# Performance work log

Hardware: AMD Instinct MI355X
Metric: run time of the kernel (lower is better)

## Reference

```python
import jax, jax.numpy as jnp
import numpy as np

GRAY_W = jnp.array([0.2989, 0.587, 0.114], dtype=jnp.float32)  # torchvision rgb_to_grayscale


def bilinear_sample(img, sx, sy):
    """img: [..., H, W]; sx, sy: [Ho, Wo] source pixel coords; zero padding (grid_sample bilinear)."""
    H, W = img.shape[-2], img.shape[-1]
    x0 = jnp.floor(sx)
    y0 = jnp.floor(sy)
    wx1 = sx - x0
    wy1 = sy - y0
    wx0 = 1.0 - wx1
    wy0 = 1.0 - wy1

    def gather(xi, yi):
        valid = (xi >= 0) & (xi <= W - 1) & (yi >= 0) & (yi <= H - 1)
        xc = jnp.clip(xi, 0, W - 1).astype(jnp.int32)
        yc = jnp.clip(yi, 0, H - 1).astype(jnp.int32)
        return img[..., yc, xc] * valid.astype(img.dtype)

    return (gather(x0, y0) * (wy0 * wx0) + gather(x0 + 1.0, y0) * (wy0 * wx1)
            + gather(x0, y0 + 1.0) * (wy1 * wx0) + gather(x0 + 1.0, y0 + 1.0) * (wy1 * wx1))


def forward(adv_patch, lab_batch, img_size):
    B, L = lab_batch.shape[0], lab_batch.shape[1]
    N, S = B * L, img_size
    key = jax.random.key(42)
    kb, kc, ks, kn, ka, ksc, kp = jax.random.split(key, 7)

    # Resize (bilinear, half-pixel centers). All N expanded copies are identical at this
    # point, so resize + color-jitter once on the single patch, then broadcast (same math).
    p = jax.image.resize(adv_patch, (3, S, S), method="bilinear")

    # ColorJitter: one factor per transform per call, applied to the whole batch.
    b = jax.random.uniform(kb, (), minval=0.8, maxval=1.1)
    c = jax.random.uniform(kc, (), minval=0.8, maxval=1.1)
    s = jax.random.uniform(ks, (), minval=0.8, maxval=1.1)
    p = p * b                                                    # brightness
    p = c * p + (1.0 - c) * jnp.einsum('chw,c->hw', p, GRAY_W).mean()   # contrast
    p = s * p + (1.0 - s) * jnp.einsum('chw,c->hw', p, GRAY_W)[None]    # saturation

    # Uniform noise in [-1,1] * noise_factor, per element of the full [N,3,S,S] batch.
    batch = p[None] + 0.15 * jax.random.uniform(kn, (N, 3, S, S), minval=-1.0, maxval=1.0)

    # RandomAffine(degrees=(-45,45), scale=(0.1,0.16)): rotation+scale about image
    # center, one sample per call; inverse map, shared [S,S] grid for all N images.
    theta = jnp.deg2rad(jax.random.uniform(ka, (), minval=-45.0, maxval=45.0))
    sc = jax.random.uniform(ksc, (), minval=0.1, maxval=0.16)
    ctr = (S - 1) / 2.0
    xs = jnp.arange(S, dtype=jnp.float32) - ctr
    dy, dx = jnp.meshgrid(xs, xs, indexing='ij')
    cos_t, sin_t = jnp.cos(theta), jnp.sin(theta)
    sx = (cos_t * dx + sin_t * dy) / sc + ctr
    sy = (-sin_t * dx + cos_t * dy) / sc + ctr
    batch = bilinear_sample(batch, sx, sy)

    # RandomPerspective(distortion_scale=0.6, p=1.0): corners pulled inward by random
    # integer offsets in [0, 0.6*half]; solve homography T with T(endpoint)=startpoint
    # (output->source map), shared for the whole batch.
    dmax = int(0.6 * (S // 2))
    r = jax.random.randint(kp, (8,), 0, dmax + 1).astype(jnp.float32)
    w = jnp.float32(S - 1)
    end = jnp.stack([jnp.stack([r[0], r[1]]),
                     jnp.stack([w - r[2], r[3]]),
                     jnp.stack([w - r[4], w - r[5]]),
                     jnp.stack([r[6], w - r[7]])])  # [4,2] endpoints (tl,tr,br,bl)
    start = jnp.array([[0.0, 0.0], [1.0, 0.0], [1.0, 1.0], [0.0, 1.0]], jnp.float32) * w
    ex, ey = end[:, 0], end[:, 1]
    px, py = start[:, 0], start[:, 1]
    z, o = jnp.zeros(4, jnp.float32), jnp.ones(4, jnp.float32)
    A = jnp.concatenate([
        jnp.stack([ex, ey, o, z, z, z, -px * ex, -px * ey], axis=1),
        jnp.stack([z, z, z, ex, ey, o, -py * ex, -py * ey], axis=1)], axis=0)  # [8,8]
    rhs = jnp.concatenate([px, py])
    h = jnp.linalg.solve(A, rhs)
    xo = jnp.arange(S, dtype=jnp.float32) + 0.5  # torchvision perspective grid offset
    yo_g, xo_g = jnp.meshgrid(xo, xo, indexing='ij')
    den = h[6] * xo_g + h[7] * yo_g + 1.0
    psx = (h[0] * xo_g + h[1] * yo_g + h[2]) / den - 0.5
    psy = (h[3] * xo_g + h[4] * yo_g + h[5]) / den - 0.5
    batch = bilinear_sample(batch, psx, psy)

    return jnp.clip(batch, 0.0, 0.99).reshape(B, L, 3, S, S)


def setup_inputs() -> dict:
    key = jax.random.key(0)
    k1, k2 = jax.random.split(key)
    return {
        "adv_patch": jax.random.uniform(k1, (3, 300, 300), dtype=jnp.float32),
        "lab_batch": jax.random.normal(k2, (8, 14, 5), dtype=jnp.float32),
        "img_size": 416,
    }


def reference(adv_patch, lab_batch, img_size):
    return forward(adv_patch, lab_batch, img_size)
```

## Files before the change

### kernel.cpp

```cpp
#include <hip/hip_runtime.h>
#include <cstdint>
#include <cstring>
#include <cmath>

__host__ __device__ static inline uint32_t rotl32(uint32_t x, int r) {
  return (x << r) | (x >> (32 - r));
}

__host__ __device__ static inline void tf2x32(uint32_t k0, uint32_t k1,
                                              uint32_t c0, uint32_t c1,
                                              uint32_t& o0, uint32_t& o1) {
  const uint32_t ks2 = 0x1BD11BDAu ^ k0 ^ k1;
  uint32_t x0 = c0 + k0;
  uint32_t x1 = c1 + k1;
#define TF_QR(r) { x0 += x1; x1 = rotl32(x1, (r)); x1 ^= x0; }
  TF_QR(13) TF_QR(15) TF_QR(26) TF_QR(6)
  x0 += k1;  x1 += ks2 + 1u;
  TF_QR(17) TF_QR(29) TF_QR(16) TF_QR(24)
  x0 += ks2; x1 += k0 + 2u;
  TF_QR(13) TF_QR(15) TF_QR(26) TF_QR(6)
  x0 += k0;  x1 += k1 + 3u;
  TF_QR(17) TF_QR(29) TF_QR(16) TF_QR(24)
  x0 += k1;  x1 += ks2 + 4u;
  TF_QR(13) TF_QR(15) TF_QR(26) TF_QR(6)
  x0 += ks2; x1 += k0 + 5u;
#undef TF_QR
  o0 = x0; o1 = x1;
}

__host__ __device__ static inline uint32_t tf_bits32(uint32_t k0, uint32_t k1, uint32_t i) {
  uint32_t a, b;
  tf2x32(k0, k1, 0u, i, a, b);
  return a ^ b;
}

__device__ static inline float noise_from_bits(uint32_t bits) {
  uint32_t fb = (bits >> 9) | 0x3f800000u;
  float f = __uint_as_float(fb) - 1.0f;
  float v = f * 2.0f - 1.0f;
  v = fmaxf(-1.0f, v);
  return 0.15f * v;
}


__global__ void __launch_bounds__(256)
k_resize(const float* __restrict__ src, float* __restrict__ p1,
         double* __restrict__ part, float bmul, int S, int inS, int SS) {
  __shared__ double sh[256];
  int t = blockIdx.x * 256 + threadIdx.x;
  double g = 0.0;
  if (t < SS) {
    int y = t / S, x = t - y * S;
    float fs = (float)inS / (float)S;
    float fy = ((float)y + 0.5f) * fs - 0.5f;
    float fx = ((float)x + 0.5f) * fs - 0.5f;
    float y0f = floorf(fy), x0f = floorf(fx);
    float ty = fy - y0f, tx = fx - x0f;
    int y0 = (int)y0f, x0 = (int)x0f;
    int y1 = y0 + 1, x1 = x0 + 1;
    y0 = min(max(y0, 0), inS - 1); y1 = min(max(y1, 0), inS - 1);
    x0 = min(max(x0, 0), inS - 1); x1 = min(max(x1, 0), inS - 1);
    float w00 = (1.f - ty) * (1.f - tx), w01 = (1.f - ty) * tx;
    float w10 = ty * (1.f - tx),         w11 = ty * tx;
    float rgb[3];
    for (int c = 0; c < 3; ++c) {
      const float* pc = src + (size_t)c * inS * inS;
      float v = pc[y0 * inS + x0] * w00 + pc[y0 * inS + x1] * w01 +
                pc[y1 * inS + x0] * w10 + pc[y1 * inS + x1] * w11;
      v *= bmul;
      p1[(size_t)c * SS + t] = v;
      rgb[c] = v;
    }
    g = (double)(0.2989f * rgb[0] + 0.587f * rgb[1] + 0.114f * rgb[2]);
  }
  sh[threadIdx.x] = g;
  __syncthreads();
  for (int s2 = 128; s2 > 0; s2 >>= 1) {
    if (threadIdx.x < s2) sh[threadIdx.x] += sh[threadIdx.x + s2];
    __syncthreads();
  }
  if (threadIdx.x == 0) part[blockIdx.x] = sh[0];
}

__global__ void __launch_bounds__(256)
k_batch1c(const float* __restrict__ p1, float* __restrict__ b1,
          const double* __restrict__ part, int nb,
          float cc, float ssat,
          uint32_t kn0, uint32_t kn1, int S, int SS, int blo, int bw, int bwp,
          float cos_t, float sin_t, float sc, float ctr) {
  __shared__ double sh[256];
  double a = 0.0;
  for (int i = threadIdx.x; i < nb; i += 256) a += part[i];
  sh[threadIdx.x] = a;
  __syncthreads();
  for (int s2 = 128; s2 > 0; s2 >>= 1) {
    if (threadIdx.x < s2) sh[threadIdx.x] += sh[threadIdx.x + s2];
    __syncthreads();
  }
  float m = (float)(sh[0] / (double)SS);

  int pix = blockIdx.x * 256 + threadIdx.x;
  if (pix >= bw * bw) return;
  int px = pix % bw;
  int py = pix / bw;
  int n  = blockIdx.y;

  int xt = blo + px, yt = blo + py;
  float dx = (float)xt - ctr, dy = (float)yt - ctr;
  float sx = (cos_t * dx + sin_t * dy) / sc + ctr;
  float sy = (-sin_t * dx + cos_t * dy) / sc + ctr;
  float x0f = floorf(sx), y0f = floorf(sy);
  float wx1 = sx - x0f, wy1 = sy - y0f;
  float wx0 = 1.f - wx1, wy0 = 1.f - wy1;
  float Wm1 = (float)(S - 1);
  float xtf[4] = {x0f, x0f + 1.f, x0f, x0f + 1.f};
  float ytf[4] = {y0f, y0f, y0f + 1.f, y0f + 1.f};
  float wt[4]  = {wy0 * wx0, wy0 * wx1, wy1 * wx0, wy1 * wx1};
  float acc[3] = {0.f, 0.f, 0.f};
  uint32_t nbase = (uint32_t)(n * 3) * (uint32_t)SS;
  float omc = 1.0f - cc, oms = 1.0f - ssat;
#pragma unroll
  for (int u = 0; u < 4; ++u) {
    bool valid = (xtf[u] >= 0.f) && (xtf[u] <= Wm1) && (ytf[u] >= 0.f) && (ytf[u] <= Wm1);
    if (!valid) continue;
    int ix = (int)xtf[u], iy = (int)ytf[u];
    int sp = iy * S + ix;
    float r = p1[sp], g = p1[SS + sp], b = p1[2 * SS + sp];
    float r2 = cc * r + omc * m;
    float g2 = cc * g + omc * m;
    float b2 = cc * b + omc * m;
    float gray = 0.2989f * r2 + 0.587f * g2 + 0.114f * b2;
    float pfv[3];
    pfv[0] = ssat * r2 + oms * gray;
    pfv[1] = ssat * g2 + oms * gray;
    pfv[2] = ssat * b2 + oms * gray;
    uint32_t idx0 = nbase + (uint32_t)sp;
#pragma unroll
    for (int c = 0; c < 3; ++c) {
      uint32_t bits = tf_bits32(kn0, kn1, idx0 + (uint32_t)(c * SS));
      acc[c] += wt[u] * (pfv[c] + noise_from_bits(bits));
    }
  }
#pragma unroll
  for (int c = 0; c < 3; ++c)
    b1[(((size_t)n * 3 + c) * bw + py) * bwp + px] = acc[c];
}

__global__ void __launch_bounds__(256)
k_out8(const float* __restrict__ b1, float4* __restrict__ out,
       int S, int X8, int blo, int bhi, int bw, int bwp, int N,
       float h0, float h1, float h2, float h3, float h4, float h5, float h6, float h7) {
  int tid = blockIdx.x * 256 + threadIdx.x;
  int total = N * S * X8;
  if (tid >= total) return;
  int x8 = tid % X8;
  int t2 = tid / X8;
  int y  = t2 % S;
  int n  = t2 / S;

  int X4 = X8 * 2;
  float yo  = (float)y + 0.5f;
  float xo0 = (float)(x8 * 8) + 0.5f;
  float xo7 = xo0 + 7.0f;

  float den0 = h6 * xo0 + h7 * yo + 1.0f;
  float den7 = h6 * xo7 + h7 * yo + 1.0f;
  float psx0 = (h0 * xo0 + h1 * yo + h2) / den0 - 0.5f;
  float psy0 = (h3 * xo0 + h4 * yo + h5) / den0 - 0.5f;
  float psx7 = (h0 * xo7 + h1 * yo + h2) / den7 - 0.5f;
  float psy7 = (h3 * xo7 + h4 * yo + h5) / den7 - 0.5f;
  float lox = fminf(psx0, psx7), hix = fmaxf(psx0, psx7);
  float loy = fminf(psy0, psy7), hiy = fmaxf(psy0, psy7);
  float bl = (float)blo - 1.5f, bh = (float)bhi + 1.5f;
  bool exterior = (den0 > 0.0f) && (den7 > 0.0f) &&
                  (hix < bl || lox > bh || hiy < bl || loy > bh);

  size_t obase = ((size_t)(n * 3) * S + y) * X4 + x8 * 2;
  size_t ostride = (size_t)S * X4;
  if (exterior) {
    float4 z = make_float4(0.f, 0.f, 0.f, 0.f);
#pragma unroll
    for (int c = 0; c < 3; ++c) {
      out[obase + (size_t)c * ostride]     = z;
      out[obase + (size_t)c * ostride + 1] = z;
    }
    return;
  }

  float acc[3][8];
#pragma unroll
  for (int c = 0; c < 3; ++c)
#pragma unroll
    for (int j = 0; j < 8; ++j) acc[c][j] = 0.f;

  float Wm1 = (float)(S - 1);
#pragma unroll
  for (int j = 0; j < 8; ++j) {
    float xo = (float)(x8 * 8 + j) + 0.5f;
    float den = h6 * xo + h7 * yo + 1.0f;
    float psx = (h0 * xo + h1 * yo + h2) / den - 0.5f;
    float psy = (h3 * xo + h4 * yo + h5) / den - 0.5f;
    float x0f = floorf(psx), y0f = floorf(psy);
    float wx1 = psx - x0f, wy1 = psy - y0f;
    float wx0 = 1.f - wx1, wy0 = 1.f - wy1;
    float xtf[4] = {x0f, x0f + 1.f, x0f, x0f + 1.f};
    float ytf[4] = {y0f, y0f, y0f + 1.f, y0f + 1.f};
    float wt[4]  = {wy0 * wx0, wy0 * wx1, wy1 * wx0, wy1 * wx1};
#pragma unroll
    for (int u = 0; u < 4; ++u) {
      bool valid = (xtf[u] >= 0.f) && (xtf[u] <= Wm1) && (ytf[u] >= 0.f) && (ytf[u] <= Wm1);
      if (!valid) continue;
      int ix = (int)xtf[u] - blo;
      int iy = (int)ytf[u] - blo;
      if (ix < 0 || ix >= bw || iy < 0 || iy >= bw) continue;
#pragma unroll
      for (int c = 0; c < 3; ++c)
        acc[c][j] += wt[u] * b1[(((size_t)n * 3 + c) * bw + iy) * bwp + ix];
    }
  }

#pragma unroll
  for (int c = 0; c < 3; ++c) {
    float4 v0, v1;
    v0.x = fminf(fmaxf(acc[c][0], 0.0f), 0.99f);
    v0.y = fminf(fmaxf(acc[c][1], 0.0f), 0.99f);
    v0.z = fminf(fmaxf(acc[c][2], 0.0f), 0.99f);
    v0.w = fminf(fmaxf(acc[c][3], 0.0f), 0.99f);
    v1.x = fminf(fmaxf(acc[c][4], 0.0f), 0.99f);
    v1.y = fminf(fmaxf(acc[c][5], 0.0f), 0.99f);
    v1.z = fminf(fmaxf(acc[c][6], 0.0f), 0.99f);
    v1.w = fminf(fmaxf(acc[c][7], 0.0f), 0.99f);
    out[obase + (size_t)c * ostride]     = v0;
    out[obase + (size_t)c * ostride + 1] = v1;
  }
}

static float bits_to_u01_host(uint32_t bits) {
  uint32_t fb = (bits >> 9) | 0x3f800000u;
  float f;
  std::memcpy(&f, &fb, 4);
  return f - 1.0f;
}

static float host_uniform(uint32_t k0, uint32_t k1, float mn, float mx) {
  uint32_t bits = tf_bits32(k0, k1, 0u);
  float f = bits_to_u01_host(bits);
  float d = mx - mn;
  float t = f * d;
  float v = t + mn;
  return v < mn ? mn : v;
}

static void solve8(float A[8][8], float b[8], float x[8]) {
  for (int k = 0; k < 8; ++k) {
    int piv = k;
    float amax = fabsf(A[k][k]);
    for (int i = k + 1; i < 8; ++i) {
      float v = fabsf(A[i][k]);
      if (v > amax) { amax = v; piv = i; }
    }
    if (piv != k) {
      for (int j = 0; j < 8; ++j) { float t = A[k][j]; A[k][j] = A[piv][j]; A[piv][j] = t; }
      float t = b[k]; b[k] = b[piv]; b[piv] = t;
    }
    for (int i = k + 1; i < 8; ++i) {
      float l = A[i][k] / A[k][k];
      A[i][k] = l;
      for (int j = k + 1; j < 8; ++j) A[i][j] -= l * A[k][j];
      b[i] -= l * b[k];
    }
  }
  for (int i = 7; i >= 0; --i) {
    float s = b[i];
    for (int j = i + 1; j < 8; ++j) s -= A[i][j] * x[j];
    x[i] = s / A[i][i];
  }
}

extern "C" void kernel_launch(void* const* d_in, const int* in_sizes, int n_in,
                              void* d_out, int out_size, void* d_ws, size_t ws_size,
                              hipStream_t stream) {
  const float* adv = (const float*)d_in[0];
  float* out = (float*)d_out;

  int inS = (int)llround(sqrt((double)in_sizes[0] / 3.0));
  int N   = in_sizes[1] / 5;
  if (N <= 0) N = 112;
  int S   = (int)llround(sqrt((double)out_size / (3.0 * N)));
  int SS  = S * S;

  uint32_t K[7][2];
  for (int i = 0; i < 7; ++i)
    tf2x32(0u, 42u, 0u, (uint32_t)i, K[i][0], K[i][1]);

  float bmul = host_uniform(K[0][0], K[0][1], 0.8f, 1.1f);
  float cc   = host_uniform(K[1][0], K[1][1], 0.8f, 1.1f);
  float ssat = host_uniform(K[2][0], K[2][1], 0.8f, 1.1f);
  float adeg = host_uniform(K[4][0], K[4][1], -45.f, 45.f);
  float theta = adeg * (float)(M_PI / 180.0);
  float sc   = host_uniform(K[5][0], K[5][1], 0.1f, 0.16f);
  float cos_t = cosf(theta), sin_t = sinf(theta);

  int dmax = (int)(0.6 * (double)(S / 2));
  uint32_t span = (uint32_t)(dmax + 1);
  uint32_t mult = ((65536u % span) * (65536u % span)) % span;
  uint32_t kp1[2], kp2[2];
  tf2x32(K[6][0], K[6][1], 0u, 0u, kp1[0], kp1[1]);
  tf2x32(K[6][0], K[6][1], 0u, 1u, kp2[0], kp2[1]);
  float r[8];
  for (int i = 0; i < 8; ++i) {
    uint32_t hi = tf_bits32(kp1[0], kp1[1], (uint32_t)i);
    uint32_t lo = tf_bits32(kp2[0], kp2[1], (uint32_t)i);
    uint32_t v = ((hi % span) * mult + (lo % span)) % span;
    r[i] = (float)v;
  }

  float w = (float)(S - 1);
  float ex[4] = {r[0], w - r[2], w - r[4], r[6]};
  float ey[4] = {r[1], r[3], w - r[5], w - r[7]};
  float px4[4] = {0.f, w, w, 0.f};
  float py4[4] = {0.f, 0.f, w, w};
  float A[8][8];
  float rhs[8];
  for (int i = 0; i < 4; ++i) {
    A[i][0] = ex[i]; A[i][1] = ey[i]; A[i][2] = 1.f;
    A[i][3] = 0.f;   A[i][4] = 0.f;   A[i][5] = 0.f;
    A[i][6] = -px4[i] * ex[i]; A[i][7] = -px4[i] * ey[i];
    rhs[i] = px4[i];
    A[4 + i][0] = 0.f; A[4 + i][1] = 0.f; A[4 + i][2] = 0.f;
    A[4 + i][3] = ex[i]; A[4 + i][4] = ey[i]; A[4 + i][5] = 1.f;
    A[4 + i][6] = -py4[i] * ex[i]; A[4 + i][7] = -py4[i] * ey[i];
    rhs[4 + i] = py4[i];
  }
  float h[8];
  solve8(A, rhs, h);

  float ctr = (float)(S - 1) * 0.5f;
  float a_half = (ctr + 2.0f) * sc;
  float bbh = a_half * (fabsf(cos_t) + fabsf(sin_t)) + 3.0f;
  int blo = (int)floorf(ctr - bbh); if (blo < 0) blo = 0;
  int bhi = (int)ceilf(ctr + bbh);  if (bhi > S - 1) bhi = S - 1;
  int bw = bhi - blo + 1;
  int bwp = (bw + 15) & ~15;

  size_t psize = (size_t)SS * 3 * sizeof(float);
  float*  p1   = (float*)d_ws;
  double* part = (double*)((char*)d_ws + psize);
  float*  b1   = (float*)((char*)d_ws + psize + 8192);

  int nb = (SS + 255) / 256;

  k_resize<<<nb, 256, 0, stream>>>(adv, p1, part, bmul, S, inS, SS);

  dim3 g3((bw * bw + 255) / 256, N);
  k_batch1c<<<g3, 256, 0, stream>>>(p1, b1, part, nb, cc, ssat,
                                    K[3][0], K[3][1], S, SS, blo, bw, bwp,
                                    cos_t, sin_t, sc, ctr);

  int X8 = S / 8;
  int totOut = N * S * X8;
  k_out8<<<(totOut + 255) / 256, 256, 0, stream>>>(
      b1, (float4*)out, S, X8, blo, bhi, bw, bwp, N,
      h[0], h[1], h[2], h[3], h[4], h[5], h[6], h[7]);
}
```

Before: 85.75 us.

## Overlap exterior zero-fill with batch build, restrict interior sampling to bounding box

The zero-filling of exterior output groups moves into the batch-building kernel as extra blocks, so those writes run alongside the noise and color-jitter work instead of in a separate pass. The host computes a conservative bounding box of non-exterior output rows and column groups, and the final warp kernel launches only over that box. This cuts the threads that only check and exit, and overlaps the large zero stores with compute. It adds a host-side scan over the grid, and correctness depends on the host-side double test being at least as conservative as the device float test.

```diff
diff --git a/kernel.cpp b/kernel.cpp
--- a/kernel.cpp
+++ b/kernel.cpp
@@ -41,7 +41,6 @@
   v = fmaxf(-1.0f, v);
   return 0.15f * v;
 }
-
 
 __global__ void __launch_bounds__(256)
 k_resize(const float* __restrict__ src, float* __restrict__ p1,
@@ -83,11 +82,49 @@
 }
 
 __global__ void __launch_bounds__(256)
-k_batch1c(const float* __restrict__ p1, float* __restrict__ b1,
-          const double* __restrict__ part, int nb,
-          float cc, float ssat,
-          uint32_t kn0, uint32_t kn1, int S, int SS, int blo, int bw, int bwp,
-          float cos_t, float sin_t, float sc, float ctr) {
+k_combined(const float* __restrict__ p1, float* __restrict__ b1,
+           const double* __restrict__ part, int nb,
+           float cc, float ssat,
+           uint32_t kn0, uint32_t kn1, int S, int SS, int blo, int bhi, int bw, int bwp,
+           float cos_t, float sin_t, float sc, float ctr, int N, int X8, int NZ,
+           float4* __restrict__ out,
+           float h0, float h1, float h2, float h3, float h4, float h5, float h6, float h7) {
+  int b = blockIdx.x;
+  if (b < NZ) {
+    int tid = b * 256 + threadIdx.x;
+    int total = N * S * X8;
+    if (tid >= total) return;
+    int x8 = tid % X8;
+    int t2 = tid / X8;
+    int y  = t2 % S;
+    int n  = t2 / S;
+    float yo  = (float)y + 0.5f;
+    float xo0 = (float)(x8 * 8) + 0.5f;
+    float xo7 = xo0 + 7.0f;
+    float den0 = h6 * xo0 + h7 * yo + 1.0f;
+    float den7 = h6 * xo7 + h7 * yo + 1.0f;
+    float psx0 = (h0 * xo0 + h1 * yo + h2) / den0 - 0.5f;
+    float psy0 = (h3 * xo0 + h4 * yo + h5) / den0 - 0.5f;
+    float psx7 = (h0 * xo7 + h1 * yo + h2) / den7 - 0.5f;
+    float psy7 = (h3 * xo7 + h4 * yo + h5) / den7 - 0.5f;
+    float lox = fminf(psx0, psx7), hix = fmaxf(psx0, psx7);
+    float loy = fminf(psy0, psy7), hiy = fmaxf(psy0, psy7);
+    float bl = (float)blo - 1.5f, bh = (float)bhi + 1.5f;
+    bool exterior = (den0 > 0.0f) && (den7 > 0.0f) &&
+                    (hix < bl || lox > bh || hiy < bl || loy > bh);
+    if (!exterior) return;
+    int X4 = X8 * 2;
+    size_t obase = ((size_t)(n * 3) * S + y) * X4 + x8 * 2;
+    size_t ostride = (size_t)S * X4;
+    float4 z = make_float4(0.f, 0.f, 0.f, 0.f);
+#pragma unroll
+    for (int c = 0; c < 3; ++c) {
+      out[obase + (size_t)c * ostride]     = z;
+      out[obase + (size_t)c * ostride + 1] = z;
+    }
+    return;
+  }
+
   __shared__ double sh[256];
   double a = 0.0;
   for (int i = threadIdx.x; i < nb; i += 256) a += part[i];
@@ -99,11 +136,12 @@
   }
   float m = (float)(sh[0] / (double)SS);
 
-  int pix = blockIdx.x * 256 + threadIdx.x;
-  if (pix >= bw * bw) return;
-  int px = pix % bw;
-  int py = pix / bw;
-  int n  = blockIdx.y;
+  int idx = (b - NZ) * 256 + threadIdx.x;
+  if (idx >= bw * bw * N) return;
+  int px = idx % bw;
+  int t2 = idx / bw;
+  int py = t2 % bw;
+  int n  = t2 / bw;
 
   int xt = blo + px, yt = blo + py;
   float dx = (float)xt - ctr, dy = (float)yt - ctr;
@@ -125,10 +163,10 @@
     if (!valid) continue;
     int ix = (int)xtf[u], iy = (int)ytf[u];
     int sp = iy * S + ix;
-    float r = p1[sp], g = p1[SS + sp], b = p1[2 * SS + sp];
+    float r = p1[sp], g = p1[SS + sp], bb = p1[2 * SS + sp];
     float r2 = cc * r + omc * m;
     float g2 = cc * g + omc * m;
-    float b2 = cc * b + omc * m;
+    float b2 = cc * bb + omc * m;
     float gray = 0.2989f * r2 + 0.587f * g2 + 0.114f * b2;
     float pfv[3];
     pfv[0] = ssat * r2 + oms * gray;
@@ -147,22 +185,21 @@
 }
 
 __global__ void __launch_bounds__(256)
-k_out8(const float* __restrict__ b1, float4* __restrict__ out,
-       int S, int X8, int blo, int bhi, int bw, int bwp, int N,
-       float h0, float h1, float h2, float h3, float h4, float h5, float h6, float h7) {
+k_out_in(const float* __restrict__ b1, float4* __restrict__ out,
+         int S, int X8, int blo, int bhi, int bw, int bwp,
+         int ylo, int rows, int glo, int gcnt, int total,
+         float h0, float h1, float h2, float h3, float h4, float h5, float h6, float h7) {
   int tid = blockIdx.x * 256 + threadIdx.x;
-  int total = N * S * X8;
   if (tid >= total) return;
-  int x8 = tid % X8;
-  int t2 = tid / X8;
-  int y  = t2 % S;
-  int n  = t2 / S;
+  int x8 = glo + tid % gcnt;
+  int t2 = tid / gcnt;
+  int y  = ylo + t2 % rows;
+  int n  = t2 / rows;
 
   int X4 = X8 * 2;
   float yo  = (float)y + 0.5f;
   float xo0 = (float)(x8 * 8) + 0.5f;
   float xo7 = xo0 + 7.0f;
-
   float den0 = h6 * xo0 + h7 * yo + 1.0f;
   float den7 = h6 * xo7 + h7 * yo + 1.0f;
   float psx0 = (h0 * xo0 + h1 * yo + h2) / den0 - 0.5f;
@@ -174,18 +211,7 @@
   float bl = (float)blo - 1.5f, bh = (float)bhi + 1.5f;
   bool exterior = (den0 > 0.0f) && (den7 > 0.0f) &&
                   (hix < bl || lox > bh || hiy < bl || loy > bh);
-
-  size_t obase = ((size_t)(n * 3) * S + y) * X4 + x8 * 2;
-  size_t ostride = (size_t)S * X4;
-  if (exterior) {
-    float4 z = make_float4(0.f, 0.f, 0.f, 0.f);
-#pragma unroll
-    for (int c = 0; c < 3; ++c) {
-      out[obase + (size_t)c * ostride]     = z;
-      out[obase + (size_t)c * ostride + 1] = z;
-    }
-    return;
-  }
+  if (exterior) return;
 
   float acc[3][8];
 #pragma unroll
@@ -219,6 +245,8 @@
     }
   }
 
+  size_t obase = ((size_t)(n * 3) * S + y) * X4 + x8 * 2;
+  size_t ostride = (size_t)S * X4;
 #pragma unroll
   for (int c = 0; c < 3; ++c) {
     float4 v0, v1;
@@ -343,6 +371,41 @@
   int bw = bhi - blo + 1;
   int bwp = (bw + 15) & ~15;
 
+  int X8 = S / 8;
+  int ylo = S, yhi = -1, glo = X8, ghi = -1;
+  {
+    double H0 = h[0], H1 = h[1], H2 = h[2], H3 = h[3], H4 = h[4], H5 = h[5], H6 = h[6], H7 = h[7];
+    double bl = (double)blo - 3.0, bh = (double)bhi + 3.0;
+    for (int y = 0; y < S; ++y) {
+      double yo = y + 0.5;
+      for (int g = 0; g < X8; ++g) {
+        double xo0 = g * 8 + 0.5, xo7 = xo0 + 7.0;
+        double den0 = H6 * xo0 + H7 * yo + 1.0;
+        double den7 = H6 * xo7 + H7 * yo + 1.0;
+        bool ext;
+        if (den0 > 0.0 && den7 > 0.0) {
+          double psx0 = (H0 * xo0 + H1 * yo + H2) / den0 - 0.5;
+          double psy0 = (H3 * xo0 + H4 * yo + H5) / den0 - 0.5;
+          double psx7 = (H0 * xo7 + H1 * yo + H2) / den7 - 0.5;
+          double psy7 = (H3 * xo7 + H4 * yo + H5) / den7 - 0.5;
+          double lox = fmin(psx0, psx7), hix = fmax(psx0, psx7);
+          double loy = fmin(psy0, psy7), hiy = fmax(psy0, psy7);
+          ext = (hix < bl || lox > bh || hiy < bl || loy > bh);
+        } else {
+          ext = false;
+        }
+        if (!ext) {
+          if (y < ylo) ylo = y;
+          if (y > yhi) yhi = y;
+          if (g < glo) glo = g;
+          if (g > ghi) ghi = g;
+        }
+      }
+    }
+  }
+  int rows = (yhi >= ylo) ? (yhi - ylo + 1) : 0;
+  int gcnt = (ghi >= glo) ? (ghi - glo + 1) : 0;
+
   size_t psize = (size_t)SS * 3 * sizeof(float);
   float*  p1   = (float*)d_ws;
   double* part = (double*)((char*)d_ws + psize);
@@ -352,14 +415,19 @@
 
   k_resize<<<nb, 256, 0, stream>>>(adv, p1, part, bmul, S, inS, SS);
 
-  dim3 g3((bw * bw + 255) / 256, N);
-  k_batch1c<<<g3, 256, 0, stream>>>(p1, b1, part, nb, cc, ssat,
-                                    K[3][0], K[3][1], S, SS, blo, bw, bwp,
-                                    cos_t, sin_t, sc, ctr);
-
-  int X8 = S / 8;
-  int totOut = N * S * X8;
-  k_out8<<<(totOut + 255) / 256, 256, 0, stream>>>(
-      b1, (float4*)out, S, X8, blo, bhi, bw, bwp, N,
+  int NZ  = (N * S * X8 + 255) / 256;
+  int NB1 = (bw * bw * N + 255) / 256;
+  k_combined<<<NZ + NB1, 256, 0, stream>>>(
+      p1, b1, part, nb, cc, ssat,
+      K[3][0], K[3][1], S, SS, blo, bhi, bw, bwp,
+      cos_t, sin_t, sc, ctr, N, X8, NZ, (float4*)out,
       h[0], h[1], h[2], h[3], h[4], h[5], h[6], h[7]);
-}
+
+  if (rows > 0 && gcnt > 0) {
+    int total = N * rows * gcnt;
+    k_out_in<<<(total + 255) / 256, 256, 0, stream>>>(
+        b1, (float4*)out, S, X8, blo, bhi, bw, bwp,
+        ylo, rows, glo, gcnt, total,
+        h[0], h[1], h[2], h[3], h[4], h[5], h[6], h[7]);
+  }
+}
```

Result: faster. 82.35 us (-4.0%).
